# Kernel tuning notes

Measured on AMD Instinct MI355X. Metric: run time of the kernel, lower is better.

Reference implementation:

```python
import jax, jax.numpy as jnp
import numpy as np

# dims: NL layers, D=d_model, DI=expand*D, F=d_ff, V=vocab, L=S*C seq, R=dt_rank, N=d_state, K=d_conv
NL, D, DI, F, V, L, R, N, K = 2, 256, 512, 1024, 1024, 1024, 16, 16, 4
B, S, C = 2, 128, 8
EPS = 1e-5


def silu(x):
    return x * jax.nn.sigmoid(x)


def batchnorm(x, g, b):  # x: [B,L,D], normalize over (B,L) per channel (training-mode BatchNorm1d)
    m = x.mean((0, 1))
    v = x.var((0, 1))
    return (x - m) * jax.lax.rsqrt(v + EPS) * g + b


def layernorm(x, g, b):
    m = x.mean(-1, keepdims=True)
    v = x.var(-1, keepdims=True)
    return (x - m) * jax.lax.rsqrt(v + EPS) * g + b


def mamba(x, Win, cw, cb, Wx, Wdt, bdt, A_log, Dsk, Wout, bout):
    # x: [B,L,D] -> [B,L,D]; standard Mamba block with selective scan
    Bsz, Lseq, _ = x.shape
    xz = x @ Win                      # [B,L,2*DI]
    xi, z = jnp.split(xz, 2, axis=-1)
    # depthwise causal conv1d, width K
    xp = jnp.pad(xi, ((0, 0), (K - 1, 0), (0, 0)))
    xc = cb + sum(xp[:, k:k + Lseq, :] * cw[:, k] for k in range(K))
    xc = silu(xc)                     # [B,L,DI]
    xdb = xc @ Wx                     # [B,L,R+2N]
    delta = jax.nn.softplus(xdb[..., :R] @ Wdt + bdt)   # [B,L,DI]
    Bm = xdb[..., R:R + N]            # [B,L,N]
    Cm = xdb[..., R + N:]             # [B,L,N]
    A = -jnp.exp(A_log)               # [DI,N]
    dA = jnp.exp(delta[..., None] * A)                       # [B,L,DI,N]
    dBx = delta[..., None] * Bm[:, :, None, :] * xc[..., None]  # [B,L,DI,N]

    def step(h, inp):
        dA_t, dBx_t, C_t = inp
        h = h * dA_t + dBx_t          # [B,DI,N]
        y = jnp.einsum('bdn,bn->bd', h, C_t)
        return h, y

    h0 = jnp.zeros((Bsz, DI, N), x.dtype)
    _, ys = jax.lax.scan(step, h0, (dA.transpose(1, 0, 2, 3), dBx.transpose(1, 0, 2, 3), Cm.transpose(1, 0, 2)))
    y = ys.transpose(1, 0, 2) + Dsk * xc
    y = y * silu(z)
    return y @ Wout + bout


def _forward(input_ids, emb, pos, Win, conv_w, conv_b, Wx, Wdt, bdt, A_log, Dskip, Wout, bout,
             bn_g, bn_b, ln_g, ln_b, ff_w1, ff_b1, ff_w2, ff_b2, final_w, final_b):
    Bsz, Ssz, Csz = input_ids.shape
    Lseq = Ssz * Csz
    # Encoder: token embedding (scaled) + learned positions, flattened to [B, S*C, D]
    x = emb[input_ids].reshape(Bsz, Lseq, D) * jnp.sqrt(jnp.float32(D)) + pos[:Lseq]
    for i in range(NL):
        f = mamba(x, Win[i, 0], conv_w[i, 0], conv_b[i, 0], Wx[i, 0], Wdt[i, 0], bdt[i, 0],
                  A_log[i, 0], Dskip[i, 0], Wout[i, 0], bout[i, 0])
        f = batchnorm(f, bn_g[i, 0], bn_b[i, 0])
        bk = mamba(x[:, ::-1], Win[i, 1], conv_w[i, 1], conv_b[i, 1], Wx[i, 1], Wdt[i, 1], bdt[i, 1],
                   A_log[i, 1], Dskip[i, 1], Wout[i, 1], bout[i, 1])
        bk = batchnorm(bk, bn_g[i, 1], bn_b[i, 1])[:, ::-1]
        f = layernorm(x + f, ln_g[i, 0], ln_b[i, 0])
        bk = layernorm(x + bk, ln_g[i, 1], ln_b[i, 1])
        out = f + bk
        out = jax.nn.relu(out @ ff_w1[i] + ff_b1[i]) @ ff_w2[i] + ff_b2[i]
        out = batchnorm(out, bn_g[i, 2], bn_b[i, 2])
        x = out + x
    return x.reshape(Bsz, Ssz, Csz, D) @ final_w + final_b   # [B,S,C,V]


def setup_inputs() -> dict:
    key = jax.random.key(0)
    ks = list(jax.random.split(key, 16))
    kit = iter(ks)
    rn = lambda shape, s=0.02: jax.random.normal(next(kit), shape, jnp.float32) * s
    inp = {
        'input_ids': jax.random.randint(next(kit), (B, S, C), 0, V),
        'emb': rn((V, D)), 'pos': rn((L, D)),
        'Win': rn((NL, 2, D, 2 * DI)),
        'conv_w': rn((NL, 2, DI, K), 0.1), 'conv_b': jnp.zeros((NL, 2, DI)),
        'Wx': rn((NL, 2, DI, R + 2 * N)),
        'Wdt': rn((NL, 2, R, DI)), 'bdt': jnp.full((NL, 2, DI), -4.0),
        'A_log': jnp.broadcast_to(jnp.log(jnp.arange(1, N + 1, dtype=jnp.float32)), (NL, 2, DI, N)) + 0.0,
        'Dskip': jnp.ones((NL, 2, DI)),
        'Wout': rn((NL, 2, DI, D)), 'bout': jnp.zeros((NL, 2, D)),
        'bn_g': jnp.ones((NL, 3, D)), 'bn_b': jnp.zeros((NL, 3, D)),
        'ln_g': jnp.ones((NL, 2, D)), 'ln_b': jnp.zeros((NL, 2, D)),
        'ff_w1': rn((NL, D, F)), 'ff_b1': jnp.zeros((NL, F)),
        'ff_w2': rn((NL, F, D)), 'ff_b2': jnp.zeros((NL, D)),
        'final_w': rn((D, V)), 'final_b': jnp.zeros((V,)),
    }
    return inp


def reference(input_ids, emb, pos, Win, conv_w, conv_b, Wx, Wdt, bdt, A_log, Dskip, Wout, bout,
              bn_g, bn_b, ln_g, ln_b, ff_w1, ff_b1, ff_w2, ff_b2, final_w, final_b):
    return _forward(input_ids, emb, pos, Win, conv_w, conv_b, Wx, Wdt, bdt, A_log, Dskip, Wout, bout,
                    bn_g, bn_b, ln_g, ln_b, ff_w1, ff_b1, ff_w2, ff_b2, final_w, final_b)
```

## Files before the change

kernel.cpp:

```cpp
#include <hip/hip_runtime.h>

#define NL 2
#define DMODEL 256
#define DI 512
#define FF 1024
#define VV 1024
#define LSEQ 1024
#define RR 16
#define NN 16
#define KCONV 4
#define BTOK 2048
#define EPS 1e-5f

using short8 = __attribute__((ext_vector_type(8))) short;
using float4v = __attribute__((ext_vector_type(4))) float;
typedef unsigned short u16;

__device__ inline float bf2f(u16 u) {
    union { unsigned u; float f; } x; x.u = (unsigned)u << 16; return x.f;
}
__device__ inline u16 f2bf(float f) {
    union { float f; unsigned u; } x; x.f = f;
    unsigned r = x.u + 0x7fffu + ((x.u >> 16) & 1u);
    return (u16)(r >> 16);
}

#if __has_builtin(__builtin_amdgcn_exp2f)
#define EXP2(x) __builtin_amdgcn_exp2f(x)
#else
#define EXP2(x) exp2f(x)
#endif

struct TMat { const float* src; u16* dst; int rows, cols, tile0, tilecols; };
struct TTable { TMat m[24]; int nmat; };

__global__ __launch_bounds__(256) void transpose_kernel(TTable tt) {
    __shared__ u16 tile[32][33];
    int bx = blockIdx.x;
    int j = 0;
    for (int k = 1; k < tt.nmat; ++k) if (bx >= tt.m[k].tile0) j = k;
    TMat mm = tt.m[j];
    int lt = bx - mm.tile0;
    int r0 = (lt / mm.tilecols) * 32, c0 = (lt % mm.tilecols) * 32;
    int tx = threadIdx.x & 31, ty = threadIdx.x >> 5;
    #pragma unroll
    for (int k = 0; k < 4; ++k) {
        int r = r0 + ty + k * 8, c = c0 + tx;
        tile[ty + k * 8][tx] = (r < mm.rows && c < mm.cols) ? f2bf(mm.src[(size_t)r * mm.cols + c]) : (u16)0;
    }
    __syncthreads();
    #pragma unroll
    for (int k = 0; k < 4; ++k) {
        int c = c0 + ty + k * 8, r = r0 + tx;
        if (c < mm.cols && r < mm.rows) mm.dst[(size_t)c * mm.rows + r] = tile[tx][ty + k * 8];
    }
}

template<int BM, int BN, int WR, int WC, int RT, int CT>
__global__ __launch_bounds__(256) void sgemm_kernel(
    const u16* __restrict__ A0, int lda, unsigned long long sA,
    const u16* __restrict__ B0, int ldb, unsigned long long sB,
    const float* __restrict__ bias0, unsigned long long sBias,
    void* __restrict__ C0, int ldc, unsigned long long sC,
    int K, int act, int outfp, float* __restrict__ stats, int statsStride)
{
    constexpr int BK = 32;
    __shared__ u16 As[BM * BK];
    __shared__ u16 Bs[BN * BK];
    const u16* A = A0 + (size_t)blockIdx.z * sA;
    const u16* Bt = B0 + (size_t)blockIdx.z * sB;
    const float* bias = bias0 ? (bias0 + (size_t)blockIdx.z * sBias) : nullptr;

    const int tid = threadIdx.x, w = tid >> 6, lane = tid & 63;
    const int row0 = blockIdx.y * BM, col0 = blockIdx.x * BN;
    const int wr = w / WC, wc = w % WC;
    const int mi = lane & 15, kq = lane >> 4;
    const int lr = lane >> 2, lc = (lane & 3) * 8;

    float4v acc[RT][CT];
    #pragma unroll
    for (int i = 0; i < RT; ++i)
        #pragma unroll
        for (int j = 0; j < CT; ++j) acc[i][j] = (float4v){0.f, 0.f, 0.f, 0.f};

    for (int kk = 0; kk < K; kk += BK) {
        __syncthreads();
        for (int i = w; i < BM / 16; i += 4) {
            const u16* g = A + (size_t)(row0 + i * 16 + lr) * lda + kk + lc;
            __builtin_amdgcn_global_load_lds(
                (const __attribute__((address_space(1))) void*)g,
                (__attribute__((address_space(3))) void*)(As + i * 16 * BK), 16, 0, 0);
        }
        for (int i = w; i < BN / 16; i += 4) {
            const u16* g = Bt + (size_t)(col0 + i * 16 + lr) * ldb + kk + lc;
            __builtin_amdgcn_global_load_lds(
                (const __attribute__((address_space(1))) void*)g,
                (__attribute__((address_space(3))) void*)(Bs + i * 16 * BK), 16, 0, 0);
        }
        __syncthreads();
        short8 af[RT], bf[CT];
        #pragma unroll
        for (int i = 0; i < RT; ++i)
            af[i] = *(const short8*)(As + (wr * RT * 16 + i * 16 + mi) * BK + kq * 8);
        #pragma unroll
        for (int j = 0; j < CT; ++j)
            bf[j] = *(const short8*)(Bs + (wc * CT * 16 + j * 16 + mi) * BK + kq * 8);
        #pragma unroll
        for (int i = 0; i < RT; ++i)
            #pragma unroll
            for (int j = 0; j < CT; ++j)
                acc[i][j] = __builtin_amdgcn_mfma_f32_16x16x32_bf16(af[i], bf[j], acc[i][j], 0, 0, 0);
    }

    #pragma unroll
    for (int j = 0; j < CT; ++j) {
        const int n = col0 + wc * CT * 16 + j * 16 + mi;
        const float bv = bias ? bias[n] : 0.f;
        float s = 0.f, q = 0.f;
        #pragma unroll
        for (int i = 0; i < RT; ++i) {
            #pragma unroll
            for (int r = 0; r < 4; ++r) {
                int m = row0 + wr * RT * 16 + i * 16 + kq * 4 + r;
                float v = acc[i][j][r] + bv;
                if (act == 1) v = fmaxf(v, 0.f);
                if (outfp)
                    ((float*)C0)[(size_t)blockIdx.z * sC + (size_t)m * ldc + n] = v;
                else
                    ((u16*)C0)[(size_t)blockIdx.z * sC + (size_t)m * ldc + n] = f2bf(v);
                s += v; q += v * v;
            }
        }
        if (stats) {
            s += __shfl_xor(s, 16); s += __shfl_xor(s, 32);
            q += __shfl_xor(q, 16); q += __shfl_xor(q, 32);
            if (lane < 16) {
                atomicAdd(&stats[(size_t)(blockIdx.z * statsStride + n) * 2], s);
                atomicAdd(&stats[(size_t)(blockIdx.z * statsStride + n) * 2 + 1], q);
            }
        }
    }
}

__global__ __launch_bounds__(256) void gemm_kernel(
    const u16* __restrict__ A0, int lda, unsigned long long sA,
    const u16* __restrict__ B0, int ldb, unsigned long long sB,
    const float* __restrict__ bias0, unsigned long long sBias,
    void* __restrict__ C0, int ldc, unsigned long long sC,
    int M, int N, int K, int act, int outfp, u16* __restrict__ bcT0)
{
    const u16* A = A0 + (size_t)blockIdx.z * sA;
    const u16* Bt = B0 + (size_t)blockIdx.z * sB;
    const float* bias = bias0 ? (bias0 + (size_t)blockIdx.z * sBias) : nullptr;

    int tid = threadIdx.x;
    int wv = tid >> 6, lane = tid & 63;
    int row0 = blockIdx.y * 64 + (wv >> 1) * 32;
    int col0 = blockIdx.x * 64 + (wv & 1) * 32;
    int mi = lane & 15, kq = lane >> 4;

    float4v acc[2][2];
    #pragma unroll
    for (int a = 0; a < 2; ++a)
        #pragma unroll
        for (int b = 0; b < 2; ++b) acc[a][b] = (float4v){0.f, 0.f, 0.f, 0.f};
    const short8 zer = {0, 0, 0, 0, 0, 0, 0, 0};

    for (int kk = 0; kk < K; kk += 32) {
        int k = kk + kq * 8;
        bool kv = (k < K);
        short8 af[2], bf[2];
        #pragma unroll
        for (int rt = 0; rt < 2; ++rt) {
            int r = row0 + rt * 16 + mi;
            af[rt] = kv ? *(const short8*)(A + (size_t)r * lda + k) : zer;
        }
        #pragma unroll
        for (int ct = 0; ct < 2; ++ct) {
            int n = col0 + ct * 16 + mi;
            bf[ct] = (kv && n < N) ? *(const short8*)(Bt + (size_t)n * ldb + k) : zer;
        }
        #pragma unroll
        for (int rt = 0; rt < 2; ++rt)
            #pragma unroll
            for (int ct = 0; ct < 2; ++ct)
                acc[rt][ct] = __builtin_amdgcn_mfma_f32_16x16x32_bf16(af[rt], bf[ct], acc[rt][ct], 0, 0, 0);
    }

    #pragma unroll
    for (int rt = 0; rt < 2; ++rt)
        #pragma unroll
        for (int ct = 0; ct < 2; ++ct) {
            int n = col0 + ct * 16 + mi;
            if (n >= N) continue;
            float bv = bias ? bias[n] : 0.f;
            #pragma unroll
            for (int r = 0; r < 4; ++r) {
                int m = row0 + rt * 16 + kq * 4 + r;
                float v = acc[rt][ct][r] + bv;
                if (act == 1) v = fmaxf(v, 0.f);
                u16 hv = f2bf(v);
                if (outfp)
                    ((float*)C0)[(size_t)blockIdx.z * sC + (size_t)m * ldc + n] = v;
                else
                    ((u16*)C0)[(size_t)blockIdx.z * sC + (size_t)m * ldc + n] = hv;
                if (bcT0 && n >= 16) {
                    int bb = m >> 10, t = m & 1023;
                    bcT0[((size_t)((blockIdx.z * 2 + bb) * 32 + (n - 16))) * LSEQ + t] = hv;
                }
            }
        }
}

__global__ __launch_bounds__(256) void delta_fused_kernel(
    const u16* __restrict__ xdb, const u16* __restrict__ wdtT,
    const float* __restrict__ bdt, const u16* __restrict__ xc,
    u16* __restrict__ deltaT, u16* __restrict__ uT, int layer)
{
    int z = blockIdx.z;
    const u16* A = xdb + (size_t)z * BTOK * 48;
    const u16* Bt = wdtT + (size_t)z * 512 * 16;
    const float* bias = bdt + (size_t)z * 512;

    int tid = threadIdx.x;
    int wv = tid >> 6, lane = tid & 63;
    int row0 = blockIdx.y * 64 + (wv >> 1) * 32;
    int col0 = blockIdx.x * 64 + (wv & 1) * 32;
    int mi = lane & 15, kq = lane >> 4;

    float4v acc[2][2];
    #pragma unroll
    for (int a = 0; a < 2; ++a)
        #pragma unroll
        for (int b = 0; b < 2; ++b) acc[a][b] = (float4v){0.f, 0.f, 0.f, 0.f};
    const short8 zer = {0, 0, 0, 0, 0, 0, 0, 0};

    int k = kq * 8;
    bool kv = (k < 16);
    short8 af[2], bf[2];
    #pragma unroll
    for (int rt = 0; rt < 2; ++rt) {
        int r = row0 + rt * 16 + mi;
        af[rt] = kv ? *(const short8*)(A + (size_t)r * 48 + k) : zer;
    }
    #pragma unroll
    for (int ct = 0; ct < 2; ++ct) {
        int n = col0 + ct * 16 + mi;
        bf[ct] = kv ? *(const short8*)(Bt + (size_t)n * 16 + k) : zer;
    }
    #pragma unroll
    for (int rt = 0; rt < 2; ++rt)
        #pragma unroll
        for (int ct = 0; ct < 2; ++ct)
            acc[rt][ct] = __builtin_amdgcn_mfma_f32_16x16x32_bf16(af[rt], bf[ct], acc[rt][ct], 0, 0, 0);

    #pragma unroll
    for (int rt = 0; rt < 2; ++rt)
        #pragma unroll
        for (int ct = 0; ct < 2; ++ct) {
            int n = col0 + ct * 16 + mi;
            float bv = bias[n];
            #pragma unroll
            for (int r = 0; r < 4; ++r) {
                int m = row0 + rt * 16 + kq * 4 + r;
                float v = acc[rt][ct][r] + bv;
                v = (v > 20.f) ? v : logf(1.f + __expf(v));
                float xcv = bf2f(xc[((size_t)z * BTOK + m) * DI + n]);
                int b = m >> 10, t = m & 1023;
                size_t off = ((size_t)((z * 2 + b) * DI + n)) * LSEQ + t;
                deltaT[off] = f2bf(v);
                uT[off] = f2bf(v * xcv);
            }
        }
}

__global__ __launch_bounds__(256) void embed_kernel(
    const int* __restrict__ ids, const float* __restrict__ emb,
    const float* __restrict__ pos, u16* __restrict__ x)
{
    int tok = blockIdx.x, d = threadIdx.x;
    int id = ids[tok];
    float v = emb[(size_t)id * DMODEL + d] * 16.0f + pos[(size_t)(tok & (LSEQ - 1)) * DMODEL + d];
    x[(size_t)tok * DMODEL + d] = f2bf(v);
}

__global__ __launch_bounds__(256) void conv_kernel(
    const u16* __restrict__ xz, const float* __restrict__ conv_w,
    const float* __restrict__ conv_b, u16* __restrict__ xc, int layer)
{
    unsigned g = blockIdx.x * 256u + threadIdx.x;
    int d = g & 511;
    int t = (g >> 9) & 1023;
    int b = (g >> 19) & 1;
    int dir = g >> 20;
    int wbase = ((layer * 2 + dir) * DI + d);
    float acc = conv_b[wbase];
    int colbase = dir * 1024 + d;
    #pragma unroll
    for (int k = 0; k < KCONV; ++k) {
        int ts = dir ? (t + 3 - k) : (t - 3 + k);
        if (ts >= 0 && ts < LSEQ)
            acc += conv_w[wbase * KCONV + k] * bf2f(xz[(size_t)((b << 10) + ts) * 2048 + colbase]);
    }
    float v = acc / (1.f + __expf(-acc));
    xc[(size_t)(((dir * 2 + b) << 10) + t) * DI + d] = f2bf(v);
}

template<int DIR>
__device__ __forceinline__ void scan_body(
    const u16* __restrict__ deltaT, const u16* __restrict__ uT,
    const u16* __restrict__ bcT, const float* __restrict__ A_log,
    u16* __restrict__ pT, int layer, int slab,
    float* Ps, float* Qs)
{
    const int c = threadIdx.x;
    const int d = blockIdx.x;

    float a2[16];
    const float* al = A_log + (size_t)(((layer * 2 + DIR) * DI + d) * NN);
    #pragma unroll
    for (int n = 0; n < 16; ++n) a2[n] = -__expf(al[n]) * 1.44269504f;

    const size_t tb = ((size_t)(slab * DI + d)) * LSEQ;
    const size_t bcb = (size_t)slab * 32 * LSEQ;
    const int T0 = DIR ? (1016 - 8 * c) : (8 * c);

    short8 dlv = *(const short8*)(deltaT + tb + T0);
    short8 uvv = *(const short8*)(uT + tb + T0);
    float dls[8], uvs[8];
    #pragma unroll
    for (int s = 0; s < 8; ++s) {
        const int idx = DIR ? 7 - s : s;
        dls[s] = bf2f((u16)dlv[idx]);
        uvs[s] = bf2f((u16)uvv[idx]);
    }

    const int base = c * 17;
    #pragma unroll
    for (int n = 0; n < 16; ++n) {
        short8 B8 = *(const short8*)(bcT + bcb + (size_t)n * LSEQ + T0);
        float P = 1.f, Q = 0.f;
        #pragma unroll
        for (int s = 0; s < 8; ++s) {
            const int idx = DIR ? 7 - s : s;
            float dA = EXP2(dls[s] * a2[n]);
            Q = Q * dA + uvs[s] * bf2f((u16)B8[idx]);
            P *= dA;
        }
        Ps[base + n] = P;
        Qs[base + n] = Q;
    }
    __syncthreads();

    for (int off = 1; off < 128; off <<= 1) {
        float np[16], nq[16];
        const bool act = (c >= off);
        if (act) {
            const int nb = (c - off) * 17;
            #pragma unroll
            for (int n = 0; n < 16; ++n) { np[n] = Ps[nb + n]; nq[n] = Qs[nb + n]; }
        }
        __syncthreads();
        if (act) {
            #pragma unroll
            for (int n = 0; n < 16; ++n) {
                float p = Ps[base + n], q = Qs[base + n];
                Qs[base + n] = fmaf(p, nq[n], q);
                Ps[base + n] = p * np[n];
            }
        }
        __syncthreads();
    }

    float pacc[8];
    #pragma unroll
    for (int s = 0; s < 8; ++s) pacc[s] = 0.f;
    const int hb = (c - 1) * 17;
    #pragma unroll
    for (int n = 0; n < 16; ++n) {
        short8 B8 = *(const short8*)(bcT + bcb + (size_t)n * LSEQ + T0);
        short8 C8 = *(const short8*)(bcT + bcb + (size_t)(16 + n) * LSEQ + T0);
        float h = (c == 0) ? 0.f : Qs[hb + n];
        #pragma unroll
        for (int s = 0; s < 8; ++s) {
            const int idx = DIR ? 7 - s : s;
            float dA = EXP2(dls[s] * a2[n]);
            h = h * dA + uvs[s] * bf2f((u16)B8[idx]);
            pacc[s] = fmaf(h, bf2f((u16)C8[idx]), pacc[s]);
        }
    }
    short8 pk;
    #pragma unroll
    for (int s = 0; s < 8; ++s) {
        const int idx = DIR ? 7 - s : s;
        pk[idx] = (short)f2bf(pacc[s]);
    }
    *(short8*)(pT + tb + T0) = pk;
}

__global__ __launch_bounds__(128) void scan_kernel(
    const u16* __restrict__ deltaT, const u16* __restrict__ uT,
    const u16* __restrict__ bcT, const float* __restrict__ A_log,
    u16* __restrict__ pT, int layer)
{
    __shared__ float Ps[128 * 17], Qs[128 * 17];
    int slab = blockIdx.y;
    if (slab >> 1)
        scan_body<1>(deltaT, uT, bcT, A_log, pT, layer, slab, Ps, Qs);
    else
        scan_body<0>(deltaT, uT, bcT, A_log, pT, layer, slab, Ps, Qs);
}

__global__ __launch_bounds__(256) void gate_kernel(
    const u16* __restrict__ pT, const u16* __restrict__ xc,
    const u16* __restrict__ xz, const float* __restrict__ Dskip,
    u16* __restrict__ y, float* __restrict__ statsM, int layer)
{
    if (blockIdx.x == 0 && blockIdx.y == 0 && blockIdx.z == 0) {
        for (int k = threadIdx.x; k < 2048; k += 256) statsM[k] = 0.f;
    }
    __shared__ float tile[32][33];
    int z = blockIdx.z, dir = z >> 1, b = z & 1;
    int d0 = blockIdx.x * 32, t0 = blockIdx.y * 32;
    int tx = threadIdx.x & 31, ty = threadIdx.x >> 5;
    #pragma unroll
    for (int k = 0; k < 4; ++k) {
        int d = d0 + ty + k * 8;
        tile[ty + k * 8][tx] = bf2f(pT[((size_t)(z * DI + d)) * LSEQ + t0 + tx]);
    }
    __syncthreads();
    #pragma unroll
    for (int k = 0; k < 4; ++k) {
        int t = t0 + ty + k * 8, d = d0 + tx;
        float p = tile[tx][ty + k * 8];
        float xcv = bf2f(xc[(size_t)((z << 10) + t) * DI + d]);
        float zv = bf2f(xz[(size_t)((b << 10) + t) * 2048 + dir * 1024 + 512 + d]);
        float dsk = Dskip[(layer * 2 + dir) * DI + d];
        float yv = (p + dsk * xcv) * (zv / (1.f + __expf(-zv)));
        y[(size_t)((z << 10) + t) * DI + d] = f2bf(yv);
    }
}

__global__ __launch_bounds__(256) void fuseln_kernel(
    const u16* __restrict__ x, const u16* __restrict__ outm, const float* __restrict__ stats,
    const float* __restrict__ bng, const float* __restrict__ bnb,
    const float* __restrict__ lng, const float* __restrict__ lnb,
    u16* __restrict__ ffin, float* __restrict__ statsF)
{
    int tok = blockIdx.x, d = threadIdx.x;
    if (tok == 0) { for (int k = d; k < 512; k += 256) statsF[k] = 0.f; }
    float xv = bf2f(x[(size_t)tok * DMODEL + d]);
    float of = bf2f(outm[(size_t)tok * DMODEL + d]);
    float ob = bf2f(outm[(size_t)BTOK * DMODEL + (size_t)tok * DMODEL + d]);
    float mf0 = stats[d * 2] * (1.f / 2048.f);
    float rf0 = rsqrtf(stats[d * 2 + 1] * (1.f / 2048.f) - mf0 * mf0 + EPS);
    float mb0 = stats[(DMODEL + d) * 2] * (1.f / 2048.f);
    float rb0 = rsqrtf(stats[(DMODEL + d) * 2 + 1] * (1.f / 2048.f) - mb0 * mb0 + EPS);
    float vf = xv + (of - mf0) * rf0 * bng[d] + bnb[d];
    float vb = xv + (ob - mb0) * rb0 * bng[DMODEL + d] + bnb[DMODEL + d];
    float s0 = vf, s1 = vf * vf, s2 = vb, s3 = vb * vb;
    #pragma unroll
    for (int off = 1; off < 64; off <<= 1) {
        s0 += __shfl_xor(s0, off); s1 += __shfl_xor(s1, off);
        s2 += __shfl_xor(s2, off); s3 += __shfl_xor(s3, off);
    }
    __shared__ float sm[4][4];
    if ((d & 63) == 0) { sm[d >> 6][0] = s0; sm[d >> 6][1] = s1; sm[d >> 6][2] = s2; sm[d >> 6][3] = s3; }
    __syncthreads();
    s0 = sm[0][0] + sm[1][0] + sm[2][0] + sm[3][0];
    s1 = sm[0][1] + sm[1][1] + sm[2][1] + sm[3][1];
    s2 = sm[0][2] + sm[1][2] + sm[2][2] + sm[3][2];
    s3 = sm[0][3] + sm[1][3] + sm[2][3] + sm[3][3];
    float mf = s0 * (1.f / 256.f), vvf = s1 * (1.f / 256.f) - mf * mf;
    float mb = s2 * (1.f / 256.f), vvb = s3 * (1.f / 256.f) - mb * mb;
    float fl = (vf - mf) * rsqrtf(vvf + EPS) * lng[d] + lnb[d];
    float bl = (vb - mb) * rsqrtf(vvb + EPS) * lng[DMODEL + d] + lnb[DMODEL + d];
    ffin[(size_t)tok * DMODEL + d] = f2bf(fl + bl);
}

__global__ __launch_bounds__(256) void bnadd_kernel(
    u16* __restrict__ x, const u16* __restrict__ ffo, const float* __restrict__ stats,
    const float* __restrict__ g, const float* __restrict__ b)
{
    int tok = blockIdx.x, d = threadIdx.x;
    size_t idx = (size_t)tok * DMODEL + d;
    float mean = stats[d * 2] * (1.f / 2048.f);
    float rs = rsqrtf(stats[d * 2 + 1] * (1.f / 2048.f) - mean * mean + EPS);
    float v = bf2f(x[idx]) + (bf2f(ffo[idx]) - mean) * rs * g[d] + b[d];
    x[idx] = f2bf(v);
}

extern "C" void kernel_launch(void* const* d_in, const int* in_sizes, int n_in,
                              void* d_out, int out_size, void* d_ws, size_t ws_size,
                              hipStream_t stream)
{
    const int*   ids     = (const int*)d_in[0];
    const float* emb     = (const float*)d_in[1];
    const float* pos     = (const float*)d_in[2];
    const float* Win     = (const float*)d_in[3];
    const float* conv_w  = (const float*)d_in[4];
    const float* conv_b  = (const float*)d_in[5];
    const float* Wx      = (const float*)d_in[6];
    const float* Wdt     = (const float*)d_in[7];
    const float* bdt     = (const float*)d_in[8];
    const float* A_log   = (const float*)d_in[9];
    const float* Dskip   = (const float*)d_in[10];
    const float* Wout    = (const float*)d_in[11];
    const float* bout    = (const float*)d_in[12];
    const float* bn_g    = (const float*)d_in[13];
    const float* bn_b    = (const float*)d_in[14];
    const float* ln_g    = (const float*)d_in[15];
    const float* ln_b    = (const float*)d_in[16];
    const float* ff_w1   = (const float*)d_in[17];
    const float* ff_b1   = (const float*)d_in[18];
    const float* ff_w2   = (const float*)d_in[19];
    const float* ff_b2   = (const float*)d_in[20];
    const float* final_w = (const float*)d_in[21];
    const float* final_b = (const float*)d_in[22];

    char* cur = (char*)d_ws;
    auto alloc = [&](size_t elems) {
        u16* p = (u16*)cur;
        cur += ((elems * 2 + 511) / 512) * 512;
        return p;
    };
    u16* winT  = alloc((size_t)NL * 2048 * 256);
    u16* wxT   = alloc((size_t)NL * 2 * 48 * 512);
    u16* wdtT  = alloc((size_t)NL * 2 * 512 * 16);
    u16* woutT = alloc((size_t)NL * 2 * 256 * 512);
    u16* fw1T  = alloc((size_t)NL * 1024 * 256);
    u16* fw2T  = alloc((size_t)NL * 256 * 1024);
    u16* finT  = alloc((size_t)1024 * 256);
    u16* xbuf   = alloc((size_t)BTOK * DMODEL);
    u16* xz     = alloc((size_t)BTOK * 2048);
    u16* xc     = alloc((size_t)2 * BTOK * DI);
    u16* xdb    = alloc((size_t)2 * BTOK * 48);
    u16* bcT    = alloc((size_t)4 * 32 * LSEQ);
    u16* deltaT = alloc((size_t)2 * BTOK * DI);
    u16* uT     = alloc((size_t)2 * BTOK * DI);
    u16* pT     = alloc((size_t)2 * BTOK * DI);
    u16* ybuf   = alloc((size_t)2 * BTOK * DI);
    u16* outm   = alloc((size_t)2 * BTOK * DMODEL);
    u16* ffin   = alloc((size_t)BTOK * DMODEL);
    u16* ffh    = alloc((size_t)BTOK * FF);
    u16* ffo    = alloc((size_t)BTOK * DMODEL);
    float* statsM = (float*)alloc(4096);
    float* statsF = statsM + 2048;

    TTable tt; int nm = 0, tiles = 0;
    auto addT = [&](const float* src, u16* dst, int rows, int cols) {
        int tc = (cols + 31) / 32, tr = (rows + 31) / 32;
        tt.m[nm] = {src, dst, rows, cols, tiles, tc};
        tiles += tc * tr; nm++;
    };
    for (int i = 0; i < NL; ++i) {
        for (int dir = 0; dir < 2; ++dir) {
            addT(Win  + (size_t)(i * 2 + dir) * 256 * 1024, winT  + (size_t)i * 2048 * 256 + (size_t)dir * 1024 * 256, 256, 1024);
            addT(Wx   + (size_t)(i * 2 + dir) * 512 * 48,   wxT   + (size_t)(i * 2 + dir) * 48 * 512,   512, 48);
            addT(Wdt  + (size_t)(i * 2 + dir) * 16 * 512,   wdtT  + (size_t)(i * 2 + dir) * 512 * 16,   16, 512);
            addT(Wout + (size_t)(i * 2 + dir) * 512 * 256,  woutT + (size_t)(i * 2 + dir) * 256 * 512,  512, 256);
        }
        addT(ff_w1 + (size_t)i * 256 * 1024, fw1T + (size_t)i * 1024 * 256, 256, 1024);
        addT(ff_w2 + (size_t)i * 1024 * 256, fw2T + (size_t)i * 256 * 1024, 1024, 256);
    }
    addT(final_w, finT, 256, 1024);
    tt.nmat = nm;
    transpose_kernel<<<tiles, 256, 0, stream>>>(tt);

    embed_kernel<<<BTOK, 256, 0, stream>>>(ids, emb, pos, xbuf);

    for (int i = 0; i < NL; ++i) {
        sgemm_kernel<128, 128, 2, 2, 4, 4><<<dim3(16, 16), 256, 0, stream>>>(
            xbuf, 256, 0ULL, winT + (size_t)i * 2048 * 256, 256, 0ULL, nullptr, 0ULL,
            xz, 2048, 0ULL, 256, 0, 0, nullptr, 0);
        conv_kernel<<<(2 * BTOK * DI) / 256, 256, 0, stream>>>(xz, conv_w, conv_b, xc, i);
        gemm_kernel<<<dim3(1, 32, 2), 256, 0, stream>>>(
            xc, 512, (unsigned long long)((size_t)BTOK * 512),
            wxT + (size_t)i * 2 * 48 * 512, 512, 48ULL * 512, nullptr, 0ULL,
            xdb, 48, (unsigned long long)((size_t)BTOK * 48), BTOK, 48, 512, 0, 0, bcT);
        delta_fused_kernel<<<dim3(8, 32, 2), 256, 0, stream>>>(
            xdb, wdtT + (size_t)i * 2 * 512 * 16, bdt + (size_t)i * 2 * 512, xc, deltaT, uT, i);
        scan_kernel<<<dim3(512, 4), 128, 0, stream>>>(deltaT, uT, bcT, A_log, pT, i);
        gate_kernel<<<dim3(DI / 32, LSEQ / 32, 4), 256, 0, stream>>>(pT, xc, xz, Dskip, ybuf, statsM, i);
        sgemm_kernel<64, 64, 2, 2, 2, 2><<<dim3(4, 32, 2), 256, 0, stream>>>(
            ybuf, 512, (unsigned long long)((size_t)BTOK * 512),
            woutT + (size_t)i * 2 * 256 * 512, 512, 256ULL * 512,
            bout + (size_t)i * 2 * 256, 256ULL,
            outm, 256, (unsigned long long)((size_t)BTOK * 256), 512, 0, 0, statsM, 256);
        fuseln_kernel<<<BTOK, 256, 0, stream>>>(xbuf, outm, statsM,
            bn_g + (size_t)i * 3 * 256, bn_b + (size_t)i * 3 * 256,
            ln_g + (size_t)i * 2 * 256, ln_b + (size_t)i * 2 * 256, ffin, statsF);
        sgemm_kernel<128, 64, 4, 1, 2, 4><<<dim3(16, 16), 256, 0, stream>>>(
            ffin, 256, 0ULL, fw1T + (size_t)i * 1024 * 256, 256, 0ULL,
            ff_b1 + (size_t)i * 1024, 0ULL, ffh, 1024, 0ULL, 256, 1, 0, nullptr, 0);
        sgemm_kernel<64, 64, 2, 2, 2, 2><<<dim3(4, 32), 256, 0, stream>>>(
            ffh, 1024, 0ULL, fw2T + (size_t)i * 256 * 1024, 1024, 0ULL,
            ff_b2 + (size_t)i * 256, 0ULL, ffo, 256, 0ULL, 1024, 0, 0, statsF, 0);
        bnadd_kernel<<<BTOK, 256, 0, stream>>>(xbuf, ffo, statsF,
            bn_g + (size_t)(i * 3 + 2) * 256, bn_b + (size_t)(i * 3 + 2) * 256);
    }
    sgemm_kernel<128, 64, 4, 1, 2, 4><<<dim3(16, 16), 256, 0, stream>>>(
        xbuf, 256, 0ULL, finT, 256, 0ULL, final_b, 0ULL,
        d_out, 1024, 0ULL, 256, 0, 1, nullptr, 0);
}
```

Before: 387.8 us.

## Fuse whole forward pass into one cooperative persistent megakernel with grid syncs

Replaces the sequence of separate kernel launches (transpose, embed, GEMMs, conv, scan, gate, norms) with a single cooperative kernel. Every phase runs as a grid-stride loop over virtual blocks, and phases are separated by grid-wide barriers. It also fuses the x-projection GEMM with the delta computation and changes several GEMM tile shapes. This removes launch overhead and inter-kernel gaps, at the cost of grid-sync latency, a fixed grid size capped by occupancy, and less freedom to tune each phase.

```diff
diff --git a/kernel.cpp b/kernel.cpp
--- a/kernel.cpp
+++ b/kernel.cpp
@@ -1,12 +1,13 @@
 #include <hip/hip_runtime.h>
+#include <hip/hip_cooperative_groups.h>
+
+namespace cg = cooperative_groups;
 
 #define NL 2
 #define DMODEL 256
 #define DI 512
 #define FF 1024
-#define VV 1024
 #define LSEQ 1024
-#define RR 16
 #define NN 16
 #define KCONV 4
 #define BTOK 2048
@@ -34,288 +35,225 @@
 struct TMat { const float* src; u16* dst; int rows, cols, tile0, tilecols; };
 struct TTable { TMat m[24]; int nmat; };
 
-__global__ __launch_bounds__(256) void transpose_kernel(TTable tt) {
-    __shared__ u16 tile[32][33];
-    int bx = blockIdx.x;
-    int j = 0;
-    for (int k = 1; k < tt.nmat; ++k) if (bx >= tt.m[k].tile0) j = k;
-    TMat mm = tt.m[j];
-    int lt = bx - mm.tile0;
-    int r0 = (lt / mm.tilecols) * 32, c0 = (lt % mm.tilecols) * 32;
+struct MegaArgs {
+    TTable tt; int ttiles;
+    const int* ids;
+    const float *emb, *pos, *conv_w, *conv_b, *A_log, *Dskip, *bdt;
+    const float *bn_g, *bn_b, *ln_g, *ln_b, *ff_b1, *ff_b2, *bout, *final_b;
+    const u16 *winT, *wxT, *wdtT, *woutT, *fw1T, *fw2T, *finT;
+    u16 *xbuf, *xz, *xc, *bcT, *deltaT, *uT, *pT, *ybuf, *outm, *ffin, *ffh, *ffo;
+    float *statsM, *statsF;
+    float* dout;
+};
+
+__device__ void transpose_phase(const TTable& tt, int ttiles, char* smem_) {
+    u16 (*tile)[33] = (u16(*)[33])smem_;
     int tx = threadIdx.x & 31, ty = threadIdx.x >> 5;
-    #pragma unroll
-    for (int k = 0; k < 4; ++k) {
-        int r = r0 + ty + k * 8, c = c0 + tx;
-        tile[ty + k * 8][tx] = (r < mm.rows && c < mm.cols) ? f2bf(mm.src[(size_t)r * mm.cols + c]) : (u16)0;
-    }
-    __syncthreads();
-    #pragma unroll
-    for (int k = 0; k < 4; ++k) {
-        int c = c0 + ty + k * 8, r = r0 + tx;
-        if (c < mm.cols && r < mm.rows) mm.dst[(size_t)c * mm.rows + r] = tile[tx][ty + k * 8];
+    for (int bx = blockIdx.x; bx < ttiles; bx += gridDim.x) {
+        __syncthreads();
+        int j = 0;
+        for (int k = 1; k < tt.nmat; ++k) if (bx >= tt.m[k].tile0) j = k;
+        TMat mm = tt.m[j];
+        int lt = bx - mm.tile0;
+        int r0 = (lt / mm.tilecols) * 32, c0 = (lt % mm.tilecols) * 32;
+        #pragma unroll
+        for (int k = 0; k < 4; ++k) {
+            int r = r0 + ty + k * 8, c = c0 + tx;
+            tile[ty + k * 8][tx] = (r < mm.rows && c < mm.cols) ? f2bf(mm.src[(size_t)r * mm.cols + c]) : (u16)0;
+        }
+        __syncthreads();
+        #pragma unroll
+        for (int k = 0; k < 4; ++k) {
+            int c = c0 + ty + k * 8, r = r0 + tx;
+            if (c < mm.cols && r < mm.rows) mm.dst[(size_t)c * mm.rows + r] = tile[tx][ty + k * 8];
+        }
+    }
+}
+
+__device__ void embed_phase(const int* ids, const float* emb, const float* pos, u16* x) {
+    int d = threadIdx.x;
+    for (int tok = blockIdx.x; tok < BTOK; tok += gridDim.x) {
+        int id = ids[tok];
+        float v = emb[(size_t)id * DMODEL + d] * 16.0f + pos[(size_t)(tok & (LSEQ - 1)) * DMODEL + d];
+        x[(size_t)tok * DMODEL + d] = f2bf(v);
     }
 }
 
 template<int BM, int BN, int WR, int WC, int RT, int CT>
-__global__ __launch_bounds__(256) void sgemm_kernel(
-    const u16* __restrict__ A0, int lda, unsigned long long sA,
-    const u16* __restrict__ B0, int ldb, unsigned long long sB,
-    const float* __restrict__ bias0, unsigned long long sBias,
-    void* __restrict__ C0, int ldc, unsigned long long sC,
-    int K, int act, int outfp, float* __restrict__ stats, int statsStride)
+__device__ void sgemm_phase(
+    const u16* A0, int lda, unsigned long long sA,
+    const u16* B0, int ldb, unsigned long long sB,
+    const float* bias0, unsigned long long sBias,
+    void* C0, int ldc, unsigned long long sC,
+    int K, int act, int outfp, float* stats, int statsStride,
+    int nbx, int nby, int nbz, char* smem_)
 {
     constexpr int BK = 32;
-    __shared__ u16 As[BM * BK];
-    __shared__ u16 Bs[BN * BK];
-    const u16* A = A0 + (size_t)blockIdx.z * sA;
-    const u16* Bt = B0 + (size_t)blockIdx.z * sB;
-    const float* bias = bias0 ? (bias0 + (size_t)blockIdx.z * sBias) : nullptr;
-
+    u16* As = (u16*)smem_;
+    u16* Bs = As + BM * BK;
     const int tid = threadIdx.x, w = tid >> 6, lane = tid & 63;
-    const int row0 = blockIdx.y * BM, col0 = blockIdx.x * BN;
     const int wr = w / WC, wc = w % WC;
     const int mi = lane & 15, kq = lane >> 4;
     const int lr = lane >> 2, lc = (lane & 3) * 8;
-
-    float4v acc[RT][CT];
-    #pragma unroll
-    for (int i = 0; i < RT; ++i)
-        #pragma unroll
-        for (int j = 0; j < CT; ++j) acc[i][j] = (float4v){0.f, 0.f, 0.f, 0.f};
-
-    for (int kk = 0; kk < K; kk += BK) {
-        __syncthreads();
-        for (int i = w; i < BM / 16; i += 4) {
-            const u16* g = A + (size_t)(row0 + i * 16 + lr) * lda + kk + lc;
-            __builtin_amdgcn_global_load_lds(
-                (const __attribute__((address_space(1))) void*)g,
-                (__attribute__((address_space(3))) void*)(As + i * 16 * BK), 16, 0, 0);
-        }
-        for (int i = w; i < BN / 16; i += 4) {
-            const u16* g = Bt + (size_t)(col0 + i * 16 + lr) * ldb + kk + lc;
-            __builtin_amdgcn_global_load_lds(
-                (const __attribute__((address_space(1))) void*)g,
-                (__attribute__((address_space(3))) void*)(Bs + i * 16 * BK), 16, 0, 0);
-        }
-        __syncthreads();
-        short8 af[RT], bf[CT];
+    const int ntiles = nbx * nby * nbz;
+    for (int vb = blockIdx.x; vb < ntiles; vb += gridDim.x) {
+        int bz = vb / (nbx * nby);
+        int rem = vb - bz * (nbx * nby);
+        int by = rem / nbx, bx = rem - by * nbx;
+        const u16* A = A0 + (size_t)bz * sA;
+        const u16* Bt = B0 + (size_t)bz * sB;
+        const float* bias = bias0 ? (bias0 + (size_t)bz * sBias) : nullptr;
+        const int row0 = by * BM, col0 = bx * BN;
+
+        float4v acc[RT][CT];
         #pragma unroll
         for (int i = 0; i < RT; ++i)
-            af[i] = *(const short8*)(As + (wr * RT * 16 + i * 16 + mi) * BK + kq * 8);
-        #pragma unroll
-        for (int j = 0; j < CT; ++j)
-            bf[j] = *(const short8*)(Bs + (wc * CT * 16 + j * 16 + mi) * BK + kq * 8);
-        #pragma unroll
-        for (int i = 0; i < RT; ++i)
+            #pragma unroll
+            for (int j = 0; j < CT; ++j) acc[i][j] = (float4v){0.f, 0.f, 0.f, 0.f};
+
+        for (int kk = 0; kk < K; kk += BK) {
+            __syncthreads();
+            for (int i = w; i < BM / 16; i += 4) {
+                const u16* g = A + (size_t)(row0 + i * 16 + lr) * lda + kk + lc;
+                __builtin_amdgcn_global_load_lds(
+                    (const __attribute__((address_space(1))) void*)g,
+                    (__attribute__((address_space(3))) void*)(As + i * 16 * BK), 16, 0, 0);
+            }
+            for (int i = w; i < BN / 16; i += 4) {
+                const u16* g = Bt + (size_t)(col0 + i * 16 + lr) * ldb + kk + lc;
+                __builtin_amdgcn_global_load_lds(
+                    (const __attribute__((address_space(1))) void*)g,
+                    (__attribute__((address_space(3))) void*)(Bs + i * 16 * BK), 16, 0, 0);
+            }
+            __syncthreads();
+            short8 af[RT], bf[CT];
+            #pragma unroll
+            for (int i = 0; i < RT; ++i)
+                af[i] = *(const short8*)(As + (wr * RT * 16 + i * 16 + mi) * BK + kq * 8);
             #pragma unroll
             for (int j = 0; j < CT; ++j)
-                acc[i][j] = __builtin_amdgcn_mfma_f32_16x16x32_bf16(af[i], bf[j], acc[i][j], 0, 0, 0);
-    }
-
-    #pragma unroll
-    for (int j = 0; j < CT; ++j) {
-        const int n = col0 + wc * CT * 16 + j * 16 + mi;
-        const float bv = bias ? bias[n] : 0.f;
-        float s = 0.f, q = 0.f;
-        #pragma unroll
-        for (int i = 0; i < RT; ++i) {
-            #pragma unroll
-            for (int r = 0; r < 4; ++r) {
-                int m = row0 + wr * RT * 16 + i * 16 + kq * 4 + r;
-                float v = acc[i][j][r] + bv;
-                if (act == 1) v = fmaxf(v, 0.f);
-                if (outfp)
-                    ((float*)C0)[(size_t)blockIdx.z * sC + (size_t)m * ldc + n] = v;
-                else
-                    ((u16*)C0)[(size_t)blockIdx.z * sC + (size_t)m * ldc + n] = f2bf(v);
-                s += v; q += v * v;
-            }
-        }
-        if (stats) {
-            s += __shfl_xor(s, 16); s += __shfl_xor(s, 32);
-            q += __shfl_xor(q, 16); q += __shfl_xor(q, 32);
-            if (lane < 16) {
-                atomicAdd(&stats[(size_t)(blockIdx.z * statsStride + n) * 2], s);
-                atomicAdd(&stats[(size_t)(blockIdx.z * statsStride + n) * 2 + 1], q);
-            }
-        }
-    }
-}
-
-__global__ __launch_bounds__(256) void gemm_kernel(
-    const u16* __restrict__ A0, int lda, unsigned long long sA,
-    const u16* __restrict__ B0, int ldb, unsigned long long sB,
-    const float* __restrict__ bias0, unsigned long long sBias,
-    void* __restrict__ C0, int ldc, unsigned long long sC,
-    int M, int N, int K, int act, int outfp, u16* __restrict__ bcT0)
-{
-    const u16* A = A0 + (size_t)blockIdx.z * sA;
-    const u16* Bt = B0 + (size_t)blockIdx.z * sB;
-    const float* bias = bias0 ? (bias0 + (size_t)blockIdx.z * sBias) : nullptr;
-
-    int tid = threadIdx.x;
-    int wv = tid >> 6, lane = tid & 63;
-    int row0 = blockIdx.y * 64 + (wv >> 1) * 32;
-    int col0 = blockIdx.x * 64 + (wv & 1) * 32;
+                bf[j] = *(const short8*)(Bs + (wc * CT * 16 + j * 16 + mi) * BK + kq * 8);
+            #pragma unroll
+            for (int i = 0; i < RT; ++i)
+                #pragma unroll
+                for (int j = 0; j < CT; ++j)
+                    acc[i][j] = __builtin_amdgcn_mfma_f32_16x16x32_bf16(af[i], bf[j], acc[i][j], 0, 0, 0);
+        }
+
+        #pragma unroll
+        for (int j = 0; j < CT; ++j) {
+            const int n = col0 + wc * CT * 16 + j * 16 + mi;
+            const float bv = bias ? bias[n] : 0.f;
+            float s = 0.f, q = 0.f;
+            #pragma unroll
+            for (int i = 0; i < RT; ++i) {
+                #pragma unroll
+                for (int r = 0; r < 4; ++r) {
+                    int m = row0 + wr * RT * 16 + i * 16 + kq * 4 + r;
+                    float v = acc[i][j][r] + bv;
+                    if (act == 1) v = fmaxf(v, 0.f);
+                    if (outfp)
+                        ((float*)C0)[(size_t)bz * sC + (size_t)m * ldc + n] = v;
+                    else
+                        ((u16*)C0)[(size_t)bz * sC + (size_t)m * ldc + n] = f2bf(v);
+                    s += v; q += v * v;
+                }
+            }
+            if (stats) {
+                s += __shfl_xor(s, 16); s += __shfl_xor(s, 32);
+                q += __shfl_xor(q, 16); q += __shfl_xor(q, 32);
+                if (lane < 16) {
+                    atomicAdd(&stats[(size_t)(bz * statsStride + n) * 2], s);
+                    atomicAdd(&stats[(size_t)(bz * statsStride + n) * 2 + 1], q);
+                }
+            }
+        }
+    }
+}
+
+__device__ void conv_phase(const u16* xz, const float* conv_w, const float* conv_b,
+                           u16* xc, int layer) {
+    for (int vb = blockIdx.x; vb < 8192; vb += gridDim.x) {
+        unsigned g = vb * 256u + threadIdx.x;
+        int d = g & 511;
+        int t = (g >> 9) & 1023;
+        int b = (g >> 19) & 1;
+        int dir = g >> 20;
+        int wbase = ((layer * 2 + dir) * DI + d);
+        float acc = conv_b[wbase];
+        int colbase = dir * 1024 + d;
+        #pragma unroll
+        for (int k = 0; k < KCONV; ++k) {
+            int ts = dir ? (t + 3 - k) : (t - 3 + k);
+            if (ts >= 0 && ts < LSEQ)
+                acc += conv_w[wbase * KCONV + k] * bf2f(xz[(size_t)((b << 10) + ts) * 2048 + colbase]);
+        }
+        float v = acc / (1.f + __expf(-acc));
+        xc[(size_t)(((dir * 2 + b) << 10) + t) * DI + d] = f2bf(v);
+    }
+}
+
+__device__ void xdb_delta_phase(const u16* xc, const u16* wxT_l, const u16* wdtT_l,
+                                const float* bdt_l, u16* bcT, u16* deltaT, u16* uT,
+                                char* smem_) {
+    u16* xdb16 = (u16*)smem_;
+    const short8 zer = {0, 0, 0, 0, 0, 0, 0, 0};
+    int w = threadIdx.x >> 6, lane = threadIdx.x & 63;
     int mi = lane & 15, kq = lane >> 4;
-
-    float4v acc[2][2];
-    #pragma unroll
-    for (int a = 0; a < 2; ++a)
-        #pragma unroll
-        for (int b = 0; b < 2; ++b) acc[a][b] = (float4v){0.f, 0.f, 0.f, 0.f};
-    const short8 zer = {0, 0, 0, 0, 0, 0, 0, 0};
-
-    for (int kk = 0; kk < K; kk += 32) {
-        int k = kk + kq * 8;
-        bool kv = (k < K);
-        short8 af[2], bf[2];
-        #pragma unroll
-        for (int rt = 0; rt < 2; ++rt) {
-            int r = row0 + rt * 16 + mi;
-            af[rt] = kv ? *(const short8*)(A + (size_t)r * lda + k) : zer;
-        }
-        #pragma unroll
-        for (int ct = 0; ct < 2; ++ct) {
-            int n = col0 + ct * 16 + mi;
-            bf[ct] = (kv && n < N) ? *(const short8*)(Bt + (size_t)n * ldb + k) : zer;
-        }
-        #pragma unroll
-        for (int rt = 0; rt < 2; ++rt)
-            #pragma unroll
-            for (int ct = 0; ct < 2; ++ct)
-                acc[rt][ct] = __builtin_amdgcn_mfma_f32_16x16x32_bf16(af[rt], bf[ct], acc[rt][ct], 0, 0, 0);
-    }
-
-    #pragma unroll
-    for (int rt = 0; rt < 2; ++rt)
-        #pragma unroll
-        for (int ct = 0; ct < 2; ++ct) {
-            int n = col0 + ct * 16 + mi;
-            if (n >= N) continue;
-            float bv = bias ? bias[n] : 0.f;
-            #pragma unroll
-            for (int r = 0; r < 4; ++r) {
-                int m = row0 + rt * 16 + kq * 4 + r;
-                float v = acc[rt][ct][r] + bv;
-                if (act == 1) v = fmaxf(v, 0.f);
-                u16 hv = f2bf(v);
-                if (outfp)
-                    ((float*)C0)[(size_t)blockIdx.z * sC + (size_t)m * ldc + n] = v;
-                else
-                    ((u16*)C0)[(size_t)blockIdx.z * sC + (size_t)m * ldc + n] = hv;
-                if (bcT0 && n >= 16) {
-                    int bb = m >> 10, t = m & 1023;
-                    bcT0[((size_t)((blockIdx.z * 2 + bb) * 32 + (n - 16))) * LSEQ + t] = hv;
-                }
-            }
-        }
-}
-
-__global__ __launch_bounds__(256) void delta_fused_kernel(
-    const u16* __restrict__ xdb, const u16* __restrict__ wdtT,
-    const float* __restrict__ bdt, const u16* __restrict__ xc,
-    u16* __restrict__ deltaT, u16* __restrict__ uT, int layer)
-{
-    int z = blockIdx.z;
-    const u16* A = xdb + (size_t)z * BTOK * 48;
-    const u16* Bt = wdtT + (size_t)z * 512 * 16;
-    const float* bias = bdt + (size_t)z * 512;
-
-    int tid = threadIdx.x;
-    int wv = tid >> 6, lane = tid & 63;
-    int row0 = blockIdx.y * 64 + (wv >> 1) * 32;
-    int col0 = blockIdx.x * 64 + (wv & 1) * 32;
-    int mi = lane & 15, kq = lane >> 4;
-
-    float4v acc[2][2];
-    #pragma unroll
-    for (int a = 0; a < 2; ++a)
-        #pragma unroll
-        for (int b = 0; b < 2; ++b) acc[a][b] = (float4v){0.f, 0.f, 0.f, 0.f};
-    const short8 zer = {0, 0, 0, 0, 0, 0, 0, 0};
-
-    int k = kq * 8;
-    bool kv = (k < 16);
-    short8 af[2], bf[2];
-    #pragma unroll
-    for (int rt = 0; rt < 2; ++rt) {
-        int r = row0 + rt * 16 + mi;
-        af[rt] = kv ? *(const short8*)(A + (size_t)r * 48 + k) : zer;
-    }
-    #pragma unroll
-    for (int ct = 0; ct < 2; ++ct) {
-        int n = col0 + ct * 16 + mi;
-        bf[ct] = kv ? *(const short8*)(Bt + (size_t)n * 16 + k) : zer;
-    }
-    #pragma unroll
-    for (int rt = 0; rt < 2; ++rt)
-        #pragma unroll
-        for (int ct = 0; ct < 2; ++ct)
-            acc[rt][ct] = __builtin_amdgcn_mfma_f32_16x16x32_bf16(af[rt], bf[ct], acc[rt][ct], 0, 0, 0);
-
-    #pragma unroll
-    for (int rt = 0; rt < 2; ++rt)
-        #pragma unroll
-        for (int ct = 0; ct < 2; ++ct) {
-            int n = col0 + ct * 16 + mi;
-            float bv = bias[n];
-            #pragma unroll
-            for (int r = 0; r < 4; ++r) {
-                int m = row0 + rt * 16 + kq * 4 + r;
-                float v = acc[rt][ct][r] + bv;
+    for (int vb = blockIdx.x; vb < 512; vb += gridDim.x) {
+        __syncthreads();
+        int dir = vb >> 8, r5 = vb & 255, tile = r5 >> 1, half = r5 & 1;
+        int m0 = tile * 16;
+        int b = m0 >> 10, tbase = m0 & 1023;
+        if (w < 3) {
+            int n = w * 16 + mi;
+            const u16* Arow = xc + ((size_t)(dir * BTOK + m0 + mi)) * 512;
+            const u16* Brow = wxT_l + (size_t)dir * 48 * 512 + (size_t)n * 512;
+            float4v acc = (float4v){0.f, 0.f, 0.f, 0.f};
+            for (int kk = 0; kk < 512; kk += 32) {
+                short8 af = *(const short8*)(Arow + kk + kq * 8);
+                short8 bf = *(const short8*)(Brow + kk + kq * 8);
+                acc = __builtin_amdgcn_mfma_f32_16x16x32_bf16(af, bf, acc, 0, 0, 0);
+            }
+            #pragma unroll
+            for (int rr = 0; rr < 4; ++rr) {
+                int m = kq * 4 + rr;
+                u16 hv = f2bf(acc[rr]);
+                if (w == 0) xdb16[m * 16 + mi] = hv;
+                else if ((half == 0 && w == 1) || (half == 1 && w == 2))
+                    bcT[((size_t)((dir * 2 + b) * 32 + (n - 16))) * 1024 + tbase + m] = hv;
+            }
+        }
+        __syncthreads();
+        short8 af = (kq < 2) ? *(const short8*)(xdb16 + mi * 16 + kq * 8) : zer;
+        const u16* wdtTd = wdtT_l + (size_t)dir * 512 * 16;
+        const float* biasd = bdt_l + (size_t)dir * 512;
+        #pragma unroll
+        for (int ct = 0; ct < 4; ++ct) {
+            int n = half * 256 + w * 64 + ct * 16 + mi;
+            short8 bf = (kq < 2) ? *(const short8*)(wdtTd + (size_t)n * 16 + kq * 8) : zer;
+            float4v acc = __builtin_amdgcn_mfma_f32_16x16x32_bf16(af, bf,
+                          (float4v){0.f, 0.f, 0.f, 0.f}, 0, 0, 0);
+            #pragma unroll
+            for (int rr = 0; rr < 4; ++rr) {
+                int m = kq * 4 + rr;
+                float v = acc[rr] + biasd[n];
                 v = (v > 20.f) ? v : logf(1.f + __expf(v));
-                float xcv = bf2f(xc[((size_t)z * BTOK + m) * DI + n]);
-                int b = m >> 10, t = m & 1023;
-                size_t off = ((size_t)((z * 2 + b) * DI + n)) * LSEQ + t;
+                float xcv = bf2f(xc[((size_t)(dir * BTOK + m0 + m)) * 512 + n]);
+                size_t off = ((size_t)((dir * 2 + b) * 512 + n)) * 1024 + tbase + m;
                 deltaT[off] = f2bf(v);
                 uT[off] = f2bf(v * xcv);
             }
         }
-}
-
-__global__ __launch_bounds__(256) void embed_kernel(
-    const int* __restrict__ ids, const float* __restrict__ emb,
-    const float* __restrict__ pos, u16* __restrict__ x)
-{
-    int tok = blockIdx.x, d = threadIdx.x;
-    int id = ids[tok];
-    float v = emb[(size_t)id * DMODEL + d] * 16.0f + pos[(size_t)(tok & (LSEQ - 1)) * DMODEL + d];
-    x[(size_t)tok * DMODEL + d] = f2bf(v);
-}
-
-__global__ __launch_bounds__(256) void conv_kernel(
-    const u16* __restrict__ xz, const float* __restrict__ conv_w,
-    const float* __restrict__ conv_b, u16* __restrict__ xc, int layer)
-{
-    unsigned g = blockIdx.x * 256u + threadIdx.x;
-    int d = g & 511;
-    int t = (g >> 9) & 1023;
-    int b = (g >> 19) & 1;
-    int dir = g >> 20;
-    int wbase = ((layer * 2 + dir) * DI + d);
-    float acc = conv_b[wbase];
-    int colbase = dir * 1024 + d;
-    #pragma unroll
-    for (int k = 0; k < KCONV; ++k) {
-        int ts = dir ? (t + 3 - k) : (t - 3 + k);
-        if (ts >= 0 && ts < LSEQ)
-            acc += conv_w[wbase * KCONV + k] * bf2f(xz[(size_t)((b << 10) + ts) * 2048 + colbase]);
-    }
-    float v = acc / (1.f + __expf(-acc));
-    xc[(size_t)(((dir * 2 + b) << 10) + t) * DI + d] = f2bf(v);
+    }
 }
 
 template<int DIR>
-__device__ __forceinline__ void scan_body(
+__device__ void scan_body(int c, int d, int slab,
     const u16* __restrict__ deltaT, const u16* __restrict__ uT,
     const u16* __restrict__ bcT, const float* __restrict__ A_log,
-    u16* __restrict__ pT, int layer, int slab,
-    float* Ps, float* Qs)
+    u16* __restrict__ pT, int layer, float* Ps, float* Qs)
 {
-    const int c = threadIdx.x;
-    const int d = blockIdx.x;
-
     float a2[16];
     const float* al = A_log + (size_t)(((layer * 2 + DIR) * DI + d) * NN);
     #pragma unroll
@@ -398,125 +336,193 @@
     *(short8*)(pT + tb + T0) = pk;
 }
 
-__global__ __launch_bounds__(128) void scan_kernel(
-    const u16* __restrict__ deltaT, const u16* __restrict__ uT,
-    const u16* __restrict__ bcT, const float* __restrict__ A_log,
-    u16* __restrict__ pT, int layer)
-{
-    __shared__ float Ps[128 * 17], Qs[128 * 17];
-    int slab = blockIdx.y;
-    if (slab >> 1)
-        scan_body<1>(deltaT, uT, bcT, A_log, pT, layer, slab, Ps, Qs);
-    else
-        scan_body<0>(deltaT, uT, bcT, A_log, pT, layer, slab, Ps, Qs);
-}
-
-__global__ __launch_bounds__(256) void gate_kernel(
-    const u16* __restrict__ pT, const u16* __restrict__ xc,
-    const u16* __restrict__ xz, const float* __restrict__ Dskip,
-    u16* __restrict__ y, float* __restrict__ statsM, int layer)
-{
-    if (blockIdx.x == 0 && blockIdx.y == 0 && blockIdx.z == 0) {
+__device__ void scan_phase(const u16* deltaT, const u16* uT, const u16* bcT,
+                           const float* A_log, u16* pT, int layer, char* smem_) {
+    float* sf = (float*)smem_;
+    int half = threadIdx.x >> 7;
+    int c = threadIdx.x & 127;
+    float* Ps = sf + half * 4352;
+    float* Qs = Ps + 2176;
+    for (int vb = blockIdx.x; vb < 1024; vb += gridDim.x) {
+        __syncthreads();
+        int pair = vb * 2 + half;
+        int slab = pair >> 9, d = pair & 511;
+        if (slab >> 1)
+            scan_body<1>(c, d, slab, deltaT, uT, bcT, A_log, pT, layer, Ps, Qs);
+        else
+            scan_body<0>(c, d, slab, deltaT, uT, bcT, A_log, pT, layer, Ps, Qs);
+    }
+}
+
+__device__ void gate_phase(const u16* pT, const u16* xc, const u16* xz,
+                           const float* Dskip, u16* y, float* statsM, int layer,
+                           char* smem_) {
+    if (blockIdx.x == 0)
         for (int k = threadIdx.x; k < 2048; k += 256) statsM[k] = 0.f;
-    }
-    __shared__ float tile[32][33];
-    int z = blockIdx.z, dir = z >> 1, b = z & 1;
-    int d0 = blockIdx.x * 32, t0 = blockIdx.y * 32;
+    float (*tile)[33] = (float(*)[33])smem_;
     int tx = threadIdx.x & 31, ty = threadIdx.x >> 5;
-    #pragma unroll
-    for (int k = 0; k < 4; ++k) {
-        int d = d0 + ty + k * 8;
-        tile[ty + k * 8][tx] = bf2f(pT[((size_t)(z * DI + d)) * LSEQ + t0 + tx]);
-    }
-    __syncthreads();
-    #pragma unroll
-    for (int k = 0; k < 4; ++k) {
-        int t = t0 + ty + k * 8, d = d0 + tx;
-        float p = tile[tx][ty + k * 8];
-        float xcv = bf2f(xc[(size_t)((z << 10) + t) * DI + d]);
-        float zv = bf2f(xz[(size_t)((b << 10) + t) * 2048 + dir * 1024 + 512 + d]);
-        float dsk = Dskip[(layer * 2 + dir) * DI + d];
-        float yv = (p + dsk * xcv) * (zv / (1.f + __expf(-zv)));
-        y[(size_t)((z << 10) + t) * DI + d] = f2bf(yv);
-    }
-}
-
-__global__ __launch_bounds__(256) void fuseln_kernel(
-    const u16* __restrict__ x, const u16* __restrict__ outm, const float* __restrict__ stats,
-    const float* __restrict__ bng, const float* __restrict__ bnb,
-    const float* __restrict__ lng, const float* __restrict__ lnb,
-    u16* __restrict__ ffin, float* __restrict__ statsF)
-{
-    int tok = blockIdx.x, d = threadIdx.x;
-    if (tok == 0) { for (int k = d; k < 512; k += 256) statsF[k] = 0.f; }
-    float xv = bf2f(x[(size_t)tok * DMODEL + d]);
-    float of = bf2f(outm[(size_t)tok * DMODEL + d]);
-    float ob = bf2f(outm[(size_t)BTOK * DMODEL + (size_t)tok * DMODEL + d]);
+    for (int vb = blockIdx.x; vb < 2048; vb += gridDim.x) {
+        __syncthreads();
+        int z = vb >> 9, rem = vb & 511;
+        int t0 = (rem >> 4) * 32, d0 = (rem & 15) * 32;
+        int dir = z >> 1, b = z & 1;
+        #pragma unroll
+        for (int k = 0; k < 4; ++k) {
+            int d = d0 + ty + k * 8;
+            tile[ty + k * 8][tx] = bf2f(pT[((size_t)(z * DI + d)) * LSEQ + t0 + tx]);
+        }
+        __syncthreads();
+        #pragma unroll
+        for (int k = 0; k < 4; ++k) {
+            int t = t0 + ty + k * 8, d = d0 + tx;
+            float p = tile[tx][ty + k * 8];
+            float xcv = bf2f(xc[(size_t)((z << 10) + t) * DI + d]);
+            float zv = bf2f(xz[(size_t)((b << 10) + t) * 2048 + dir * 1024 + 512 + d]);
+            float dsk = Dskip[(layer * 2 + dir) * DI + d];
+            float yv = (p + dsk * xcv) * (zv / (1.f + __expf(-zv)));
+            y[(size_t)((z << 10) + t) * DI + d] = f2bf(yv);
+        }
+    }
+}
+
+__device__ void fuseln_phase(const u16* x, const u16* outm, const float* stats,
+                             const float* bng, const float* bnb,
+                             const float* lng, const float* lnb,
+                             u16* ffin, float* statsF, char* smem_) {
+    if (blockIdx.x == 0)
+        for (int k = threadIdx.x; k < 512; k += 256) statsF[k] = 0.f;
+    float* sm = (float*)smem_;
+    int d = threadIdx.x;
     float mf0 = stats[d * 2] * (1.f / 2048.f);
     float rf0 = rsqrtf(stats[d * 2 + 1] * (1.f / 2048.f) - mf0 * mf0 + EPS);
     float mb0 = stats[(DMODEL + d) * 2] * (1.f / 2048.f);
     float rb0 = rsqrtf(stats[(DMODEL + d) * 2 + 1] * (1.f / 2048.f) - mb0 * mb0 + EPS);
-    float vf = xv + (of - mf0) * rf0 * bng[d] + bnb[d];
-    float vb = xv + (ob - mb0) * rb0 * bng[DMODEL + d] + bnb[DMODEL + d];
-    float s0 = vf, s1 = vf * vf, s2 = vb, s3 = vb * vb;
-    #pragma unroll
-    for (int off = 1; off < 64; off <<= 1) {
-        s0 += __shfl_xor(s0, off); s1 += __shfl_xor(s1, off);
-        s2 += __shfl_xor(s2, off); s3 += __shfl_xor(s3, off);
-    }
-    __shared__ float sm[4][4];
-    if ((d & 63) == 0) { sm[d >> 6][0] = s0; sm[d >> 6][1] = s1; sm[d >> 6][2] = s2; sm[d >> 6][3] = s3; }
-    __syncthreads();
-    s0 = sm[0][0] + sm[1][0] + sm[2][0] + sm[3][0];
-    s1 = sm[0][1] + sm[1][1] + sm[2][1] + sm[3][1];
-    s2 = sm[0][2] + sm[1][2] + sm[2][2] + sm[3][2];
-    s3 = sm[0][3] + sm[1][3] + sm[2][3] + sm[3][3];
-    float mf = s0 * (1.f / 256.f), vvf = s1 * (1.f / 256.f) - mf * mf;
-    float mb = s2 * (1.f / 256.f), vvb = s3 * (1.f / 256.f) - mb * mb;
-    float fl = (vf - mf) * rsqrtf(vvf + EPS) * lng[d] + lnb[d];
-    float bl = (vb - mb) * rsqrtf(vvb + EPS) * lng[DMODEL + d] + lnb[DMODEL + d];
-    ffin[(size_t)tok * DMODEL + d] = f2bf(fl + bl);
-}
-
-__global__ __launch_bounds__(256) void bnadd_kernel(
-    u16* __restrict__ x, const u16* __restrict__ ffo, const float* __restrict__ stats,
-    const float* __restrict__ g, const float* __restrict__ b)
-{
-    int tok = blockIdx.x, d = threadIdx.x;
-    size_t idx = (size_t)tok * DMODEL + d;
+    float gf = bng[d], gb = bng[DMODEL + d], bf_ = bnb[d], bb_ = bnb[DMODEL + d];
+    float lgf = lng[d], lgb = lng[DMODEL + d], lbf = lnb[d], lbb = lnb[DMODEL + d];
+    for (int tok = blockIdx.x; tok < BTOK; tok += gridDim.x) {
+        __syncthreads();
+        float xv = bf2f(x[(size_t)tok * DMODEL + d]);
+        float of = bf2f(outm[(size_t)tok * DMODEL + d]);
+        float ob = bf2f(outm[(size_t)BTOK * DMODEL + (size_t)tok * DMODEL + d]);
+        float vf = xv + (of - mf0) * rf0 * gf + bf_;
+        float vb = xv + (ob - mb0) * rb0 * gb + bb_;
+        float s0 = vf, s1 = vf * vf, s2 = vb, s3 = vb * vb;
+        #pragma unroll
+        for (int off = 1; off < 64; off <<= 1) {
+            s0 += __shfl_xor(s0, off); s1 += __shfl_xor(s1, off);
+            s2 += __shfl_xor(s2, off); s3 += __shfl_xor(s3, off);
+        }
+        if ((d & 63) == 0) {
+            sm[(d >> 6) * 4] = s0; sm[(d >> 6) * 4 + 1] = s1;
+            sm[(d >> 6) * 4 + 2] = s2; sm[(d >> 6) * 4 + 3] = s3;
+        }
+        __syncthreads();
+        s0 = sm[0] + sm[4] + sm[8] + sm[12];
+        s1 = sm[1] + sm[5] + sm[9] + sm[13];
+        s2 = sm[2] + sm[6] + sm[10] + sm[14];
+        s3 = sm[3] + sm[7] + sm[11] + sm[15];
+        float mf = s0 * (1.f / 256.f), vvf = s1 * (1.f / 256.f) - mf * mf;
+        float mb = s2 * (1.f / 256.f), vvb = s3 * (1.f / 256.f) - mb * mb;
+        float fl = (vf - mf) * rsqrtf(vvf + EPS) * lgf + lbf;
+        float bl = (vb - mb) * rsqrtf(vvb + EPS) * lgb + lbb;
+        ffin[(size_t)tok * DMODEL + d] = f2bf(fl + bl);
+    }
+}
+
+__device__ void bnadd_phase(u16* x, const u16* ffo, const float* stats,
+                            const float* g, const float* b) {
+    int d = threadIdx.x;
     float mean = stats[d * 2] * (1.f / 2048.f);
     float rs = rsqrtf(stats[d * 2 + 1] * (1.f / 2048.f) - mean * mean + EPS);
-    float v = bf2f(x[idx]) + (bf2f(ffo[idx]) - mean) * rs * g[d] + b[d];
-    x[idx] = f2bf(v);
+    float gv = g[d], bv = b[d];
+    for (int tok = blockIdx.x; tok < BTOK; tok += gridDim.x) {
+        size_t idx = (size_t)tok * DMODEL + d;
+        float v = bf2f(x[idx]) + (bf2f(ffo[idx]) - mean) * rs * gv + bv;
+        x[idx] = f2bf(v);
+    }
+}
+
+__global__ __launch_bounds__(256, 2) void mega_kernel(MegaArgs a) {
+    cg::grid_group gg = cg::this_grid();
+    __shared__ alignas(16) char smem[34816];
+
+    transpose_phase(a.tt, a.ttiles, smem);
+    embed_phase(a.ids, a.emb, a.pos, a.xbuf);
+    gg.sync();
+
+    for (int i = 0; i < NL; ++i) {
+        sgemm_phase<128, 64, 4, 1, 2, 4>(a.xbuf, 256, 0ULL,
+            a.winT + (size_t)i * 2048 * 256, 256, 0ULL, nullptr, 0ULL,
+            a.xz, 2048, 0ULL, 256, 0, 0, nullptr, 0, 32, 16, 1, smem);
+        gg.sync();
+        conv_phase(a.xz, a.conv_w, a.conv_b, a.xc, i);
+        gg.sync();
+        xdb_delta_phase(a.xc, a.wxT + (size_t)i * 2 * 48 * 512,
+            a.wdtT + (size_t)i * 2 * 512 * 16, a.bdt + (size_t)i * 2 * 512,
+            a.bcT, a.deltaT, a.uT, smem);
+        gg.sync();
+        scan_phase(a.deltaT, a.uT, a.bcT, a.A_log, a.pT, i, smem);
+        gg.sync();
+        gate_phase(a.pT, a.xc, a.xz, a.Dskip, a.ybuf, a.statsM, i, smem);
+        gg.sync();
+        sgemm_phase<64, 64, 2, 2, 2, 2>(a.ybuf, 512, (unsigned long long)BTOK * 512,
+            a.woutT + (size_t)i * 2 * 256 * 512, 512, 256ULL * 512,
+            a.bout + (size_t)i * 2 * 256, 256ULL,
+            a.outm, 256, (unsigned long long)BTOK * 256, 512, 0, 0,
+            a.statsM, 256, 4, 32, 2, smem);
+        gg.sync();
+        fuseln_phase(a.xbuf, a.outm, a.statsM,
+            a.bn_g + (size_t)i * 3 * 256, a.bn_b + (size_t)i * 3 * 256,
+            a.ln_g + (size_t)i * 2 * 256, a.ln_b + (size_t)i * 2 * 256,
+            a.ffin, a.statsF, smem);
+        gg.sync();
+        sgemm_phase<64, 64, 2, 2, 2, 2>(a.ffin, 256, 0ULL,
+            a.fw1T + (size_t)i * 1024 * 256, 256, 0ULL,
+            a.ff_b1 + (size_t)i * 1024, 0ULL,
+            a.ffh, 1024, 0ULL, 256, 1, 0, nullptr, 0, 16, 32, 1, smem);
+        gg.sync();
+        sgemm_phase<32, 64, 2, 2, 1, 2>(a.ffh, 1024, 0ULL,
+            a.fw2T + (size_t)i * 256 * 1024, 1024, 0ULL,
+            a.ff_b2 + (size_t)i * 256, 0ULL,
+            a.ffo, 256, 0ULL, 1024, 0, 0, a.statsF, 0, 4, 64, 1, smem);
+        gg.sync();
+        bnadd_phase(a.xbuf, a.ffo, a.statsF,
+            a.bn_g + (size_t)(i * 3 + 2) * 256, a.bn_b + (size_t)(i * 3 + 2) * 256);
+        gg.sync();
+    }
+    sgemm_phase<64, 64, 2, 2, 2, 2>(a.xbuf, 256, 0ULL, a.finT, 256, 0ULL,
+        a.final_b, 0ULL, a.dout, 1024, 0ULL, 256, 0, 1, nullptr, 0, 16, 32, 1, smem);
 }
 
 extern "C" void kernel_launch(void* const* d_in, const int* in_sizes, int n_in,
                               void* d_out, int out_size, void* d_ws, size_t ws_size,
                               hipStream_t stream)
 {
-    const int*   ids     = (const int*)d_in[0];
-    const float* emb     = (const float*)d_in[1];
-    const float* pos     = (const float*)d_in[2];
-    const float* Win     = (const float*)d_in[3];
-    const float* conv_w  = (const float*)d_in[4];
-    const float* conv_b  = (const float*)d_in[5];
-    const float* Wx      = (const float*)d_in[6];
-    const float* Wdt     = (const float*)d_in[7];
-    const float* bdt     = (const float*)d_in[8];
-    const float* A_log   = (const float*)d_in[9];
-    const float* Dskip   = (const float*)d_in[10];
-    const float* Wout    = (const float*)d_in[11];
-    const float* bout    = (const float*)d_in[12];
-    const float* bn_g    = (const float*)d_in[13];
-    const float* bn_b    = (const float*)d_in[14];
-    const float* ln_g    = (const float*)d_in[15];
-    const float* ln_b    = (const float*)d_in[16];
-    const float* ff_w1   = (const float*)d_in[17];
-    const float* ff_b1   = (const float*)d_in[18];
-    const float* ff_w2   = (const float*)d_in[19];
-    const float* ff_b2   = (const float*)d_in[20];
+    MegaArgs a;
+    a.ids     = (const int*)d_in[0];
+    a.emb     = (const float*)d_in[1];
+    a.pos     = (const float*)d_in[2];
+    const float* Win    = (const float*)d_in[3];
+    a.conv_w  = (const float*)d_in[4];
+    a.conv_b  = (const float*)d_in[5];
+    const float* Wx     = (const float*)d_in[6];
+    const float* Wdt    = (const float*)d_in[7];
+    a.bdt     = (const float*)d_in[8];
+    a.A_log   = (const float*)d_in[9];
+    a.Dskip   = (const float*)d_in[10];
+    const float* Wout   = (const float*)d_in[11];
+    a.bout    = (const float*)d_in[12];
+    a.bn_g    = (const float*)d_in[13];
+    a.bn_b    = (const float*)d_in[14];
+    a.ln_g    = (const float*)d_in[15];
+    a.ln_b    = (const float*)d_in[16];
+    const float* ff_w1  = (const float*)d_in[17];
+    a.ff_b1   = (const float*)d_in[18];
+    const float* ff_w2  = (const float*)d_in[19];
+    a.ff_b2   = (const float*)d_in[20];
     const float* final_w = (const float*)d_in[21];
-    const float* final_b = (const float*)d_in[22];
+    a.final_b = (const float*)d_in[22];
+    a.dout    = (float*)d_out;
 
     char* cur = (char*)d_ws;
     auto alloc = [&](size_t elems) {
@@ -531,26 +537,27 @@
     u16* fw1T  = alloc((size_t)NL * 1024 * 256);
     u16* fw2T  = alloc((size_t)NL * 256 * 1024);
     u16* finT  = alloc((size_t)1024 * 256);
-    u16* xbuf   = alloc((size_t)BTOK * DMODEL);
-    u16* xz     = alloc((size_t)BTOK * 2048);
-    u16* xc     = alloc((size_t)2 * BTOK * DI);
-    u16* xdb    = alloc((size_t)2 * BTOK * 48);
-    u16* bcT    = alloc((size_t)4 * 32 * LSEQ);
-    u16* deltaT = alloc((size_t)2 * BTOK * DI);
-    u16* uT     = alloc((size_t)2 * BTOK * DI);
-    u16* pT     = alloc((size_t)2 * BTOK * DI);
-    u16* ybuf   = alloc((size_t)2 * BTOK * DI);
-    u16* outm   = alloc((size_t)2 * BTOK * DMODEL);
-    u16* ffin   = alloc((size_t)BTOK * DMODEL);
-    u16* ffh    = alloc((size_t)BTOK * FF);
-    u16* ffo    = alloc((size_t)BTOK * DMODEL);
-    float* statsM = (float*)alloc(4096);
-    float* statsF = statsM + 2048;
-
-    TTable tt; int nm = 0, tiles = 0;
+    a.winT = winT; a.wxT = wxT; a.wdtT = wdtT; a.woutT = woutT;
+    a.fw1T = fw1T; a.fw2T = fw2T; a.finT = finT;
+    a.xbuf   = alloc((size_t)BTOK * DMODEL);
+    a.xz     = alloc((size_t)BTOK * 2048);
+    a.xc     = alloc((size_t)2 * BTOK * DI);
+    a.bcT    = alloc((size_t)4 * 32 * LSEQ);
+    a.deltaT = alloc((size_t)2 * BTOK * DI);
+    a.uT     = alloc((size_t)2 * BTOK * DI);
+    a.pT     = alloc((size_t)2 * BTOK * DI);
+    a.ybuf   = alloc((size_t)2 * BTOK * DI);
+    a.outm   = alloc((size_t)2 * BTOK * DMODEL);
+    a.ffin   = alloc((size_t)BTOK * DMODEL);
+    a.ffh    = alloc((size_t)BTOK * FF);
+    a.ffo    = alloc((size_t)BTOK * DMODEL);
+    a.statsM = (float*)alloc(8192);
+    a.statsF = a.statsM + 2048;
+
+    int nm = 0, tiles = 0;
     auto addT = [&](const float* src, u16* dst, int rows, int cols) {
         int tc = (cols + 31) / 32, tr = (rows + 31) / 32;
-        tt.m[nm] = {src, dst, rows, cols, tiles, tc};
+        a.tt.m[nm] = {src, dst, rows, cols, tiles, tc};
         tiles += tc * tr; nm++;
     };
     for (int i = 0; i < NL; ++i) {
@@ -564,42 +571,18 @@
         addT(ff_w2 + (size_t)i * 1024 * 256, fw2T + (size_t)i * 256 * 1024, 1024, 256);
     }
     addT(final_w, finT, 256, 1024);
-    tt.nmat = nm;
-    transpose_kernel<<<tiles, 256, 0, stream>>>(tt);
-
-    embed_kernel<<<BTOK, 256, 0, stream>>>(ids, emb, pos, xbuf);
-
-    for (int i = 0; i < NL; ++i) {
-        sgemm_kernel<128, 128, 2, 2, 4, 4><<<dim3(16, 16), 256, 0, stream>>>(
-            xbuf, 256, 0ULL, winT + (size_t)i * 2048 * 256, 256, 0ULL, nullptr, 0ULL,
-            xz, 2048, 0ULL, 256, 0, 0, nullptr, 0);
-        conv_kernel<<<(2 * BTOK * DI) / 256, 256, 0, stream>>>(xz, conv_w, conv_b, xc, i);
-        gemm_kernel<<<dim3(1, 32, 2), 256, 0, stream>>>(
-            xc, 512, (unsigned long long)((size_t)BTOK * 512),
-            wxT + (size_t)i * 2 * 48 * 512, 512, 48ULL * 512, nullptr, 0ULL,
-            xdb, 48, (unsigned long long)((size_t)BTOK * 48), BTOK, 48, 512, 0, 0, bcT);
-        delta_fused_kernel<<<dim3(8, 32, 2), 256, 0, stream>>>(
-            xdb, wdtT + (size_t)i * 2 * 512 * 16, bdt + (size_t)i * 2 * 512, xc, deltaT, uT, i);
-        scan_kernel<<<dim3(512, 4), 128, 0, stream>>>(deltaT, uT, bcT, A_log, pT, i);
-        gate_kernel<<<dim3(DI / 32, LSEQ / 32, 4), 256, 0, stream>>>(pT, xc, xz, Dskip, ybuf, statsM, i);
-        sgemm_kernel<64, 64, 2, 2, 2, 2><<<dim3(4, 32, 2), 256, 0, stream>>>(
-            ybuf, 512, (unsigned long long)((size_t)BTOK * 512),
-            woutT + (size_t)i * 2 * 256 * 512, 512, 256ULL * 512,
-            bout + (size_t)i * 2 * 256, 256ULL,
-            outm, 256, (unsigned long long)((size_t)BTOK * 256), 512, 0, 0, statsM, 256);
-        fuseln_kernel<<<BTOK, 256, 0, stream>>>(xbuf, outm, statsM,
-            bn_g + (size_t)i * 3 * 256, bn_b + (size_t)i * 3 * 256,
-            ln_g + (size_t)i * 2 * 256, ln_b + (size_t)i * 2 * 256, ffin, statsF);
-        sgemm_kernel<128, 64, 4, 1, 2, 4><<<dim3(16, 16), 256, 0, stream>>>(
-            ffin, 256, 0ULL, fw1T + (size_t)i * 1024 * 256, 256, 0ULL,
-            ff_b1 + (size_t)i * 1024, 0ULL, ffh, 1024, 0ULL, 256, 1, 0, nullptr, 0);
-        sgemm_kernel<64, 64, 2, 2, 2, 2><<<dim3(4, 32), 256, 0, stream>>>(
-            ffh, 1024, 0ULL, fw2T + (size_t)i * 256 * 1024, 1024, 0ULL,
-            ff_b2 + (size_t)i * 256, 0ULL, ffo, 256, 0ULL, 1024, 0, 0, statsF, 0);
-        bnadd_kernel<<<BTOK, 256, 0, stream>>>(xbuf, ffo, statsF,
-            bn_g + (size_t)(i * 3 + 2) * 256, bn_b + (size_t)(i * 3 + 2) * 256);
-    }
-    sgemm_kernel<128, 64, 4, 1, 2, 4><<<dim3(16, 16), 256, 0, stream>>>(
-        xbuf, 256, 0ULL, finT, 256, 0ULL, final_b, 0ULL,
-        d_out, 1024, 0ULL, 256, 0, 1, nullptr, 0);
-}
+    a.tt.nmat = nm;
+    a.ttiles = tiles;
+
+    int dev = 0;
+    hipGetDevice(&dev);
+    int nb = 0, cus = 0;
+    hipOccupancyMaxActiveBlocksPerMultiprocessor(&nb, (const void*)mega_kernel, 256, 0);
+    hipDeviceGetAttribute(&cus, hipDeviceAttributeMultiprocessorCount, dev);
+    int grid = 512;
+    if (nb > 0 && cus > 0 && nb * cus < grid) grid = nb * cus;
+
+    void* kargs[1] = { &a };
+    hipLaunchCooperativeKernel((void*)mega_kernel, dim3(grid), dim3(256),
+                               kargs, 0, stream);
+}
```

After: 1.264 ms. 3.26x slower.
